# Performance work log

Hardware: AMD Instinct MI355X
Metric: run time of the kernel (lower is better)

The kernel has to match this reference:

```python
import jax, jax.numpy as jnp
import numpy as np

EMBED_DIM = 512
HEADS = 8
ATTN_DIM = EMBED_DIM // HEADS
PF_DIM = 2048
B, L = 4, 2048
LN_EPS = 1e-5


def _linear(x, W, b):
    # nn.Linear: x @ W.T + b, W is [out, in]
    return jnp.einsum('bld,od->blo', x, W) + b


def _layer_norm(x, g, b):
    mu = jnp.mean(x, axis=-1, keepdims=True)
    var = jnp.mean(jnp.square(x - mu), axis=-1, keepdims=True)
    return (x - mu) * jax.lax.rsqrt(var + LN_EPS) * g + b


def _qkv(src, Wq, bq, Wk, bk, Wv, bv):
    def split(t):
        Bb, Ll, _ = t.shape
        return t.reshape(Bb, Ll, HEADS, ATTN_DIM).transpose(0, 2, 1, 3)  # [B,H,L,Dh]
    return (split(_linear(src, Wq, bq)),
            split(_linear(src, Wk, bk)),
            split(_linear(src, Wv, bv)))


def _attention(inp, Q, K1, K2, V1, V2, Wo, bo, ln_g, ln_b, W1, b1, W2, b2):
    # non-softmax linear attention: (Q K1^T) V1 + (Q K2^T) V2
    attn = (jnp.einsum('bhqk,bhkd->bhqd', jnp.einsum('bhqd,bhkd->bhqk', Q, K1), V1)
            + jnp.einsum('bhqk,bhkd->bhqd', jnp.einsum('bhqd,bhkd->bhqk', Q, K2), V2))
    Bb = Q.shape[0]
    attn = attn.transpose(0, 2, 1, 3).reshape(Bb, -1, HEADS * ATTN_DIM)  # [B,L,D]
    x = _linear(attn, Wo, bo)
    x = _layer_norm(inp + x, ln_g, ln_b)          # dropout p=0 (eval)
    ff = _linear(jax.nn.relu(_linear(x, W1, b1)), W2, b2)
    x = _layer_norm(x + ff, ln_g, ln_b)
    return x


def setup_inputs() -> dict:
    key = jax.random.key(0)
    ks = jax.random.split(key, 16)
    s = 0.02
    return {
        'question': jax.random.normal(ks[0], (B, L, EMBED_DIM), jnp.float32),
        'query': jax.random.normal(ks[1], (B, L, EMBED_DIM), jnp.float32),
        'Wq': jax.random.normal(ks[2], (EMBED_DIM, EMBED_DIM), jnp.float32) * s,
        'bq': jnp.zeros((EMBED_DIM,), jnp.float32),
        'Wk': jax.random.normal(ks[3], (EMBED_DIM, EMBED_DIM), jnp.float32) * s,
        'bk': jnp.zeros((EMBED_DIM,), jnp.float32),
        'Wv': jax.random.normal(ks[4], (EMBED_DIM, EMBED_DIM), jnp.float32) * s,
        'bv': jnp.zeros((EMBED_DIM,), jnp.float32),
        'Wo': jax.random.normal(ks[5], (EMBED_DIM, EMBED_DIM), jnp.float32) * s,
        'bo': jnp.zeros((EMBED_DIM,), jnp.float32),
        'ln_g': jnp.ones((EMBED_DIM,), jnp.float32),
        'ln_b': jnp.zeros((EMBED_DIM,), jnp.float32),
        'W1': jax.random.normal(ks[6], (PF_DIM, EMBED_DIM), jnp.float32) * s,
        'b1': jnp.zeros((PF_DIM,), jnp.float32),
        'W2': jax.random.normal(ks[7], (EMBED_DIM, PF_DIM), jnp.float32) * s,
        'b2': jnp.zeros((EMBED_DIM,), jnp.float32),
    }


def reference(question, query, Wq, bq, Wk, bk, Wv, bv, Wo, bo, ln_g, ln_b, W1, b1, W2, b2):
    Q1, K1, V1 = _qkv(question, Wq, bq, Wk, bk, Wv, bv)
    Q2, K2, V2 = _qkv(query, Wq, bq, Wk, bk, Wv, bv)
    question_attn = _attention(question, Q1, K1, K2, V1, V2, Wo, bo, ln_g, ln_b, W1, b1, W2, b2)
    query_attn = _attention(query, Q2, K2, K1, V2, V1, Wo, bo, ln_g, ln_b, W1, b1, W2, b2)
    return jnp.concatenate([question_attn, query_attn], axis=-1)
```

## Files before the change

### kernel.cpp

```cpp
#include <hip/hip_runtime.h>
#include <stdint.h>


#define Bq 4
#define Lq 2048
#define Dq 512
#define PFq 2048
#define Mrows 16384
#define MiBu 1048576ull
#define NSLICE 16

typedef __attribute__((ext_vector_type(8))) short frag_ab;
typedef __attribute__((ext_vector_type(4))) float frag_cd;
typedef __attribute__((ext_vector_type(8))) unsigned short ushort8v;

__device__ __forceinline__ unsigned short f2b(float f) {
    union { float f; uint32_t u; } x; x.f = f;
    uint32_t r = x.u + 0x7fffu + ((x.u >> 16) & 1u);
    return (unsigned short)(r >> 16);
}
__device__ __forceinline__ float b2f(unsigned short u) {
    union { uint32_t u; float f; } x; x.u = ((uint32_t)u) << 16;
    return x.f;
}

#define GLD16(g, l)                                                              \
    __builtin_amdgcn_global_load_lds(                                            \
        (const __attribute__((address_space(1))) void*)(const void*)(g),         \
        (__attribute__((address_space(3))) void*)(void*)(l), 16, 0, 0)


#define STG(BUFOFS, REGOFS, GB, ROWOFS, TILE)                                    \
    { GLD16((GB) + (size_t)(ROWOFS) * 512 + (TILE) * 64,                         \
            Sh + (BUFOFS) + (REGOFS) + ld);                                      \
      GLD16((GB) + ((size_t)(ROWOFS) + 64) * 512 + (TILE) * 64,                  \
            Sh + (BUFOFS) + (REGOFS) + ld + 4096); }

#define VMW(N) asm volatile("s_waitcnt vmcnt(" #N ")" ::: "memory")

#define PHASE(CB, M0, LOADB, STAGE_STMT, WAIT_STMT)                              \
    {                                                                            \
        frag_ab a00 = *(const frag_ab*)&Sh[(CB) + (wm + (M0)*16 + lr) * 64 + xo0];      \
        frag_ab a01 = *(const frag_ab*)&Sh[(CB) + (wm + (M0)*16 + lr) * 64 + xo1];      \
        frag_ab a10 = *(const frag_ab*)&Sh[(CB) + (wm + (M0)*16 + 16 + lr) * 64 + xo0]; \
        frag_ab a11 = *(const frag_ab*)&Sh[(CB) + (wm + (M0)*16 + 16 + lr) * 64 + xo1]; \
        if (LOADB) {                                                             \
            _Pragma("unroll")                                                    \
            for (int j = 0; j < 4; ++j) {                                        \
                bf[j][0] = *(const frag_ab*)&Sh[(CB) + 16384 + (wn + j*16 + lr)*64 + xo0]; \
                bf[j][1] = *(const frag_ab*)&Sh[(CB) + 16384 + (wn + j*16 + lr)*64 + xo1]; \
            }                                                                    \
        }                                                                        \
        STAGE_STMT;                                                              \
        WAIT_STMT;                                                               \
        __builtin_amdgcn_sched_barrier(0);                                       \
        __builtin_amdgcn_s_barrier();                                            \
        asm volatile("s_waitcnt lgkmcnt(0)" ::: "memory");                       \
        __builtin_amdgcn_sched_barrier(0);                                       \
        __builtin_amdgcn_s_setprio(1);                                           \
        _Pragma("unroll")                                                        \
        for (int j = 0; j < 4; ++j) {                                            \
            acc[(M0)][j]   = __builtin_amdgcn_mfma_f32_16x16x32_bf16(a00, bf[j][0], acc[(M0)][j], 0,0,0);   \
            acc[(M0)][j]   = __builtin_amdgcn_mfma_f32_16x16x32_bf16(a01, bf[j][1], acc[(M0)][j], 0,0,0);   \
            acc[(M0)+1][j] = __builtin_amdgcn_mfma_f32_16x16x32_bf16(a10, bf[j][0], acc[(M0)+1][j], 0,0,0); \
            acc[(M0)+1][j] = __builtin_amdgcn_mfma_f32_16x16x32_bf16(a11, bf[j][1], acc[(M0)+1][j], 0,0,0); \
        }                                                                        \
        __builtin_amdgcn_s_setprio(0);                                           \
        __builtin_amdgcn_sched_barrier(0);                                       \
        __builtin_amdgcn_s_barrier();                                            \
        __builtin_amdgcn_sched_barrier(0);                                       \
    }

__global__ __launch_bounds__(512, 2) void gemm_256(
    const unsigned short* __restrict__ A, const unsigned short* __restrict__ Wt,
    const float* __restrict__ bias, unsigned short* __restrict__ outB,
    int M, int N, int relu)
{
    __shared__ __align__(16) unsigned short Sh[65536];
    const int tid = threadIdx.x;
    const int lane = tid & 63;
    const int w = tid >> 6;
    const int wm = (w >> 2) * 128;
    const int wn = (w & 3) * 64;
    const int lr = lane & 15;
    const int quad = lane >> 4;
    const int xo0 = ((quad ^ (lr & 7)) << 3);
    const int xo1 = (((4 | quad) ^ (lr & 7)) << 3);

    const int nwg = gridDim.x;
    const int b0 = blockIdx.x;
    const int bid = (b0 & 7) * (nwg >> 3) + (b0 >> 3);
    const int mb = M >> 8;
    const size_t bm = (size_t)(bid % mb) * 256;
    const size_t bn = (size_t)(bid / mb) * 256;

    const int ar = tid >> 3;
    const int sw = ((tid & 7) ^ (ar & 7)) << 3;
    const unsigned short* Ag = A  + (bm + ar) * (size_t)512 + sw;
    const unsigned short* Bg = Wt + (bn + ar) * (size_t)512 + sw;
    const int ld = tid * 8;

    frag_cd acc[8][4] = {};
    frag_ab bf[4][2];

    STG(0,     16384, Bg, 0,   0);
    STG(0,     24576, Bg, 128, 0);
    STG(0,     0,     Ag, 0,   0);
    STG(0,     8192,  Ag, 128, 0);
    STG(32768, 16384, Bg, 0,   1);
    STG(32768, 24576, Bg, 128, 1);
    VMW(4);
    __builtin_amdgcn_sched_barrier(0);
    __builtin_amdgcn_s_barrier();
    __builtin_amdgcn_sched_barrier(0);

    for (int I = 0; I < 3; ++I) {
        const int tb = 2 * I + 1, tc = 2 * I + 2, td = 2 * I + 3;
        PHASE(0,     0, 1, STG(32768, 0,     Ag, 0,   tb), (void)0);
        PHASE(0,     2, 0, STG(32768, 8192,  Ag, 128, tb), (void)0);
        PHASE(0,     4, 0, STG(0,     16384, Bg, 0,   tc), (void)0);
        PHASE(0,     6, 0, STG(0,     24576, Bg, 128, tc), VMW(4));
        PHASE(32768, 0, 1, STG(0,     0,     Ag, 0,   tc), (void)0);
        PHASE(32768, 2, 0, STG(0,     8192,  Ag, 128, tc), (void)0);
        PHASE(32768, 4, 0, STG(32768, 16384, Bg, 0,   td), (void)0);
        PHASE(32768, 6, 0, STG(32768, 24576, Bg, 128, td), VMW(4));
    }
    PHASE(0,     0, 1, STG(32768, 0,    Ag, 0,   7), (void)0);
    PHASE(0,     2, 0, STG(32768, 8192, Ag, 128, 7), (void)0);
    PHASE(0,     4, 0, (void)0, (void)0);
    PHASE(0,     6, 0, (void)0, VMW(0));
    PHASE(32768, 0, 1, (void)0, (void)0);
    PHASE(32768, 2, 0, (void)0, (void)0);
    PHASE(32768, 4, 0, (void)0, (void)0);
    PHASE(32768, 6, 0, (void)0, (void)0);

    float bv[4];
#pragma unroll
    for (int j = 0; j < 4; ++j) bv[j] = bias[(int)bn + wn + j * 16 + lr];
    unsigned short* Cs = Sh + w * 8192;
#pragma unroll
    for (int m = 0; m < 8; ++m)
#pragma unroll
        for (int j = 0; j < 4; ++j)
#pragma unroll
            for (int r = 0; r < 4; ++r) {
                float v = acc[m][j][r] + bv[j];
                if (relu) v = fmaxf(v, 0.f);
                Cs[(m * 16 + quad * 4 + r) * 64 + j * 16 + lr] = f2b(v);
            }
    const int rl = lane >> 3, c8 = (lane & 7) * 8;
#pragma unroll
    for (int k = 0; k < 16; ++k) {
        const int row = rl + k * 8;
        ushort8v val = *(const ushort8v*)&Cs[row * 64 + c8];
        *(ushort8v*)(outB + (size_t)(bm + wm + row) * N + bn + wn + c8) = val;
    }
}

__global__ __launch_bounds__(256) void gemm_res(
    const unsigned short* __restrict__ A, const unsigned short* __restrict__ Wt,
    const float* __restrict__ bias,
    const float* __restrict__ resA, const float* __restrict__ resB,
    unsigned short* __restrict__ outB, int M, int N, int K)
{
    __shared__ __align__(16) unsigned short Sh[128 * 64 + 64 * 64];
    unsigned short* At = Sh;
    unsigned short* Bt = Sh + 128 * 64;
    const int tid = threadIdx.x;
    const int lane = tid & 63;
    const int w = tid >> 6;
    const int wm = w * 32;
    const int lr = lane & 15;
    const int quad = lane >> 4;
    const size_t bm = (size_t)blockIdx.x * 128, bn = (size_t)blockIdx.y * 64;

    frag_cd acc[2][4] = {};

    const int ar = tid >> 3;
    const int acs = (((tid & 7) ^ (ar & 7)) << 3);
    const unsigned short* Ag = A  + (bm + ar) * (size_t)K + acs;
    const unsigned short* Bg = Wt + (bn + ar) * (size_t)K + acs;
    unsigned short* Asd = At + w * 512;
    unsigned short* Bsd = Bt + w * 512;

    for (int k0 = 0; k0 < K; k0 += 64) {
        __syncthreads();
#pragma unroll
        for (int i = 0; i < 4; ++i)
            GLD16(Ag + (size_t)(32 * i) * K + k0, Asd + i * 2048);
#pragma unroll
        for (int i = 0; i < 2; ++i)
            GLD16(Bg + (size_t)(32 * i) * K + k0, Bsd + i * 2048);
        __syncthreads();
#pragma unroll
        for (int kk = 0; kk < 2; ++kk) {
            frag_ab a[2], b[4];
#pragma unroll
            for (int i = 0; i < 2; ++i)
                a[i] = *(const frag_ab*)&At[(wm + i * 16 + lr) * 64 +
                                            ((((kk << 2) | quad) ^ (lr & 7)) << 3)];
#pragma unroll
            for (int j = 0; j < 4; ++j)
                b[j] = *(const frag_ab*)&Bt[(j * 16 + lr) * 64 +
                                            ((((kk << 2) | quad) ^ (lr & 7)) << 3)];
#pragma unroll
            for (int i = 0; i < 2; ++i)
#pragma unroll
                for (int j = 0; j < 4; ++j)
                    acc[i][j] = __builtin_amdgcn_mfma_f32_16x16x32_bf16(a[i], b[j], acc[i][j], 0, 0, 0);
        }
    }

    __syncthreads();
    unsigned short* Cs = Sh + w * 2048;
#pragma unroll
    for (int j = 0; j < 4; ++j) {
        const float bv = bias[(int)bn + j * 16 + lr];
#pragma unroll
        for (int i = 0; i < 2; ++i)
#pragma unroll
            for (int r = 0; r < 4; ++r)
                Cs[(i * 16 + quad * 4 + r) * 64 + j * 16 + lr] = f2b(acc[i][j][r] + bv);
    }
    const int rl = lane >> 3;
    const int c8 = (lane & 7) * 8;
#pragma unroll
    for (int k = 0; k < 4; ++k) {
        const int row = rl + k * 8;
        const int grow = (int)bm + wm + row;
        const size_t idx = (size_t)grow * N + bn + c8;
        ushort8v val = *(const ushort8v*)&Cs[row * 64 + c8];
        float vv[8];
#pragma unroll
        for (int t = 0; t < 8; ++t) vv[t] = b2f(val[t]);
        if (resA) {
            const float* rp = (grow < 8192) ? resA + idx : resB + idx - (size_t)8192 * N;
            float4 ra = *(const float4*)(rp);
            float4 rb = *(const float4*)(rp + 4);
            vv[0] += ra.x; vv[1] += ra.y; vv[2] += ra.z; vv[3] += ra.w;
            vv[4] += rb.x; vv[5] += rb.y; vv[6] += rb.z; vv[7] += rb.w;
        } else {
            ushort8v old = *(const ushort8v*)(outB + idx);
#pragma unroll
            for (int t = 0; t < 8; ++t) vv[t] += b2f(old[t]);
        }
        ushort8v o;
#pragma unroll
        for (int t = 0; t < 8; ++t) o[t] = f2b(vv[t]);
        *(ushort8v*)(outB + idx) = o;
    }
}

__global__ __launch_bounds__(256) void convert_all(
    const float* __restrict__ Wq, const float* __restrict__ Wk,
    const float* __restrict__ Wv, const float* __restrict__ Wo,
    const float* __restrict__ W1, const float* __restrict__ W2,
    const float* __restrict__ question, const float* __restrict__ query,
    const float* __restrict__ bqp, const float* __restrict__ bkp,
    const float* __restrict__ bvp,
    unsigned short* __restrict__ Wqkvb, unsigned short* __restrict__ Wob,
    unsigned short* __restrict__ W1b, unsigned short* __restrict__ W2b,
    unsigned short* __restrict__ Xb, float* __restrict__ bqkv)
{
    const int b = blockIdx.x;
    const float* src; unsigned short* dst; size_t off;
    if (b < 256)        { src = Wq; dst = Wqkvb;          off = (size_t)b * 1024; }
    else if (b < 512)   { src = Wk; dst = Wqkvb + 262144; off = (size_t)(b - 256) * 1024; }
    else if (b < 768)   { src = Wv; dst = Wqkvb + 524288; off = (size_t)(b - 512) * 1024; }
    else if (b < 1024)  { src = Wo; dst = Wob;            off = (size_t)(b - 768) * 1024; }
    else if (b < 2048)  { src = W1; dst = W1b;            off = (size_t)(b - 1024) * 1024; }
    else if (b < 3072)  { src = W2; dst = W2b;            off = (size_t)(b - 2048) * 1024; }
    else if (b < 7168)  { src = question; dst = Xb;       off = (size_t)(b - 3072) * 1024; }
    else if (b < 11264) { src = query; dst = Xb + 4194304; off = (size_t)(b - 7168) * 1024; }
    else {
        const int n = (b - 11264) * 256 + threadIdx.x;
        bqkv[n] = (n < 512) ? bqp[n] : (n < 1024) ? bkp[n - 512] : bvp[n - 1024];
        return;
    }
    const size_t idx = off + threadIdx.x * 4;
    float4 v = *(const float4*)(src + idx);
    ushort4 o;
    o.x = f2b(v.x); o.y = f2b(v.y); o.z = f2b(v.z); o.w = f2b(v.w);
    *(ushort4*)(dst + idx) = o;
}

__global__ __launch_bounds__(256) void s_kernel(
    const unsigned short* __restrict__ QKV, float* __restrict__ Spart)
{
    const int bh = blockIdx.x;
    const int sl = blockIdx.y;
    const int b = bh >> 3, h = bh & 7;
    const int pass = sl >> 3;
    const int l0 = (sl & 7) * 256;
    __shared__ float Ks[64][64];
    __shared__ float Vs[64][64];
    const int tid = threadIdx.x;
    const int tx = tid & 15, ty = tid >> 4;
    const int srow = tid >> 3;
    const int scol = (tid & 7) * 8;
    const size_t rowbase = (size_t)pass * 8192 + (size_t)b * Lq + l0;

    float acc[4][4] = {};

    for (int t0 = 0; t0 < 256; t0 += 64) {
        const unsigned short* kp0 = QKV + (rowbase + t0 + srow) * 1536 + 512 + h * 64 + scol;
        const unsigned short* kp1 = kp0 + (size_t)32 * 1536;
        ushort8v k0 = *(const ushort8v*)kp0;
        ushort8v v0 = *(const ushort8v*)(kp0 + 512);
        ushort8v k1 = *(const ushort8v*)kp1;
        ushort8v v1 = *(const ushort8v*)(kp1 + 512);
        __syncthreads();
#pragma unroll
        for (int e = 0; e < 8; ++e) {
            Ks[srow][scol + e]      = b2f(k0[e]);
            Vs[srow][scol + e]      = b2f(v0[e]);
            Ks[srow + 32][scol + e] = b2f(k1[e]);
            Vs[srow + 32][scol + e] = b2f(v1[e]);
        }
        __syncthreads();
#pragma unroll 4
        for (int rr = 0; rr < 64; ++rr) {
            const float4 kf = *(const float4*)&Ks[rr][ty * 4];
            const float4 vf = *(const float4*)&Vs[rr][tx * 4];
            acc[0][0] = fmaf(kf.x, vf.x, acc[0][0]);
            acc[0][1] = fmaf(kf.x, vf.y, acc[0][1]);
            acc[0][2] = fmaf(kf.x, vf.z, acc[0][2]);
            acc[0][3] = fmaf(kf.x, vf.w, acc[0][3]);
            acc[1][0] = fmaf(kf.y, vf.x, acc[1][0]);
            acc[1][1] = fmaf(kf.y, vf.y, acc[1][1]);
            acc[1][2] = fmaf(kf.y, vf.z, acc[1][2]);
            acc[1][3] = fmaf(kf.y, vf.w, acc[1][3]);
            acc[2][0] = fmaf(kf.z, vf.x, acc[2][0]);
            acc[2][1] = fmaf(kf.z, vf.y, acc[2][1]);
            acc[2][2] = fmaf(kf.z, vf.z, acc[2][2]);
            acc[2][3] = fmaf(kf.z, vf.w, acc[2][3]);
            acc[3][0] = fmaf(kf.w, vf.x, acc[3][0]);
            acc[3][1] = fmaf(kf.w, vf.y, acc[3][1]);
            acc[3][2] = fmaf(kf.w, vf.z, acc[3][2]);
            acc[3][3] = fmaf(kf.w, vf.w, acc[3][3]);
        }
    }

    float* Sp = Spart + ((size_t)bh * NSLICE + sl) * 4096;
#pragma unroll
    for (int i = 0; i < 4; ++i) {
        float4 o = make_float4(acc[i][0], acc[i][1], acc[i][2], acc[i][3]);
        *(float4*)(Sp + (ty * 4 + i) * 64 + tx * 4) = o;
    }
}

__global__ __launch_bounds__(256) void sbt_convert(
    const float* __restrict__ Spart, unsigned short* __restrict__ Sbt)
{
    const int bh = blockIdx.x;
    const int uo = blockIdx.y;
    const float* Sp = Spart + (size_t)bh * (NSLICE * 4096);
    unsigned short* Dp = Sbt + (size_t)bh * 4096;
    const int t = threadIdx.x;
#pragma unroll
    for (int u = 0; u < 4; ++u) {
        const int d = (uo * 4 + u) * 256 + t;
        float v = 0.f;
#pragma unroll
        for (int s = 0; s < NSLICE; ++s) v += Sp[(size_t)s * 4096 + d];
        const int row = d >> 6, col = d & 63;
        Dp[(row >> 5) * 2048 + col * 32 + (row & 31)] = f2b(v);
    }
}

__global__ __launch_bounds__(256) void attn_mfma(
    const unsigned short* __restrict__ QKV, const unsigned short* __restrict__ Sbt,
    unsigned short* __restrict__ Ob)
{
    __shared__ __align__(16) unsigned short Sh[2 * 128 * 32 + 2 * 64 * 32];
    unsigned short* At = Sh;
    unsigned short* Bt = Sh + 2 * 128 * 32;
    const int h = blockIdx.x;
    const int rbase = blockIdx.y * 128;
    const int b = (rbase >> 11) & 3;
    const int bh = b * 8 + h;
    const int tid = threadIdx.x;
    const int lane = tid & 63;
    const int w = tid >> 6;
    const int lr = lane & 15;
    const int quad = lane >> 4;

    {
        const int rloc = tid >> 2, c8 = (tid & 3) * 8;
#pragma unroll
        for (int it = 0; it < 4; ++it) {
            const int kk = it & 1, rh = it >> 1;
            const unsigned short* g = QKV +
                ((size_t)rbase + rh * 64 + rloc) * 1536 + h * 64 + kk * 32 + c8;
            GLD16(g, At + kk * 4096 + rh * 2048 + w * 512);
        }
        const unsigned short* Sg = Sbt + (size_t)bh * 4096 + tid * 8;
#pragma unroll
        for (int bi = 0; bi < 2; ++bi)
            GLD16(Sg + bi * 2048, Bt + bi * 2048 + w * 512);
    }
    __syncthreads();

    frag_cd acc[2][4] = {};
#pragma unroll
    for (int kk = 0; kk < 2; ++kk) {
        frag_ab a[2], bfr[4];
#pragma unroll
        for (int i = 0; i < 2; ++i)
            a[i] = *(const frag_ab*)&At[kk * 4096 + (w * 32 + i * 16 + lr) * 32 + quad * 8];
#pragma unroll
        for (int j = 0; j < 4; ++j)
            bfr[j] = *(const frag_ab*)&Bt[kk * 2048 + (j * 16 + lr) * 32 + quad * 8];
#pragma unroll
        for (int i = 0; i < 2; ++i)
#pragma unroll
            for (int j = 0; j < 4; ++j)
                acc[i][j] = __builtin_amdgcn_mfma_f32_16x16x32_bf16(a[i], bfr[j], acc[i][j], 0, 0, 0);
    }

    __syncthreads();
    unsigned short* Cs = Sh + w * 2048;
#pragma unroll
    for (int i = 0; i < 2; ++i)
#pragma unroll
        for (int j = 0; j < 4; ++j)
#pragma unroll
            for (int r = 0; r < 4; ++r)
                Cs[(i * 16 + quad * 4 + r) * 64 + j * 16 + lr] = f2b(acc[i][j][r]);
    const int rl = lane >> 3;
    const int c8o = (lane & 7) * 8;
#pragma unroll
    for (int k = 0; k < 4; ++k) {
        const int row = rl + k * 8;
        ushort8v val = *(const ushort8v*)&Cs[row * 64 + c8o];
        *(ushort8v*)(Ob + (size_t)(rbase + w * 32 + row) * 512 + h * 64 + c8o) = val;
    }
}

__global__ __launch_bounds__(256) void ln_b16_inplace(
    unsigned short* __restrict__ Y, const float* __restrict__ g,
    const float* __restrict__ bta)
{
    __shared__ float part[8];
    const int row = blockIdx.x;
    const int t = threadIdx.x;
    const int w = t >> 6;
    unsigned short* yr = Y + (size_t)row * Dq;
    const float v0 = b2f(yr[t]), v1 = b2f(yr[t + 256]);
    float s = v0 + v1;
#pragma unroll
    for (int off = 32; off; off >>= 1) s += __shfl_xor(s, off, 64);
    if ((t & 63) == 0) part[w] = s;
    __syncthreads();
    const float mean = (part[0] + part[1] + part[2] + part[3]) * (1.f / Dq);
    const float d0 = v0 - mean, d1 = v1 - mean;
    float q = d0 * d0 + d1 * d1;
#pragma unroll
    for (int off = 32; off; off >>= 1) q += __shfl_xor(q, off, 64);
    if ((t & 63) == 0) part[4 + w] = q;
    __syncthreads();
    const float rstd = rsqrtf((part[4] + part[5] + part[6] + part[7]) * (1.f / Dq) + 1e-5f);
    yr[t] = f2b(d0 * rstd * g[t] + bta[t]);
    yr[t + 256] = f2b(d1 * rstd * g[t + 256] + bta[t + 256]);
}

__global__ __launch_bounds__(256) void ln_b16_out(
    const unsigned short* __restrict__ Y, const float* __restrict__ g,
    const float* __restrict__ bta, float* __restrict__ out)
{
    __shared__ float part[8];
    const int row = blockIdx.x;
    const int t = threadIdx.x;
    const int w = t >> 6;
    const unsigned short* yr = Y + (size_t)row * Dq;
    const float v0 = b2f(yr[t]), v1 = b2f(yr[t + 256]);
    float s = v0 + v1;
#pragma unroll
    for (int off = 32; off; off >>= 1) s += __shfl_xor(s, off, 64);
    if ((t & 63) == 0) part[w] = s;
    __syncthreads();
    const float mean = (part[0] + part[1] + part[2] + part[3]) * (1.f / Dq);
    const float d0 = v0 - mean, d1 = v1 - mean;
    float q = d0 * d0 + d1 * d1;
#pragma unroll
    for (int off = 32; off; off >>= 1) q += __shfl_xor(q, off, 64);
    if ((t & 63) == 0) part[4 + w] = q;
    __syncthreads();
    const float rstd = rsqrtf((part[4] + part[5] + part[6] + part[7]) * (1.f / Dq) + 1e-5f);
    const int half = row >> 13, br = row & 8191;
    float* orow = out + (size_t)br * 1024 + half * 512;
    orow[t] = d0 * rstd * g[t] + bta[t];
    orow[t + 256] = d1 * rstd * g[t + 256] + bta[t + 256];
}

extern "C" void kernel_launch(void* const* d_in, const int* in_sizes, int n_in,
                              void* d_out, int out_size, void* d_ws, size_t ws_size,
                              hipStream_t stream)
{
    const float* question = (const float*)d_in[0];
    const float* query    = (const float*)d_in[1];
    const float* Wq = (const float*)d_in[2];  const float* bqp = (const float*)d_in[3];
    const float* Wk = (const float*)d_in[4];  const float* bkp = (const float*)d_in[5];
    const float* Wv = (const float*)d_in[6];  const float* bvp = (const float*)d_in[7];
    const float* Wo = (const float*)d_in[8];  const float* bo  = (const float*)d_in[9];
    const float* ln_g = (const float*)d_in[10]; const float* ln_b = (const float*)d_in[11];
    const float* W1 = (const float*)d_in[12]; const float* b1 = (const float*)d_in[13];
    const float* W2 = (const float*)d_in[14]; const float* b2 = (const float*)d_in[15];
    float* out = (float*)d_out;
    char* ws = (char*)d_ws;

    unsigned short* QKVb  = (unsigned short*)(ws);
    unsigned short* attnb = (unsigned short*)(ws + 48 * MiBu);
    float* Spart          = (float*)(ws + 48 * MiBu);
    unsigned short* Xb    = (unsigned short*)(ws + 64 * MiBu);
    unsigned short* xbuf  = (unsigned short*)(ws + 64 * MiBu);
    unsigned short* hb    = (unsigned short*)(ws);
    char* wp = ws + 80 * MiBu + 524288;
    unsigned short* Wqkvb = (unsigned short*)wp;  wp += 1536 * 512 * 2;
    unsigned short* Wob   = (unsigned short*)wp;  wp += 512 * 512 * 2;
    unsigned short* W1b   = (unsigned short*)wp;  wp += 2048 * 512 * 2;
    unsigned short* W2b   = (unsigned short*)wp;  wp += 512 * 2048 * 2;
    unsigned short* Sbt   = (unsigned short*)wp;  wp += 32 * 4096 * 2;
    float* bqkv           = (float*)wp;

    dim3 blk(256);

    convert_all<<<11270, blk, 0, stream>>>(Wq, Wk, Wv, Wo, W1, W2, question, query,
                                           bqp, bkp, bvp,
                                           Wqkvb, Wob, W1b, W2b, Xb, bqkv);

    gemm_256<<<dim3(384), dim3(512), 0, stream>>>(Xb, Wqkvb, bqkv, QKVb,
                                                  Mrows, 1536, 0);

    s_kernel<<<dim3(32, NSLICE), blk, 0, stream>>>(QKVb, Spart);
    sbt_convert<<<dim3(32, 4), blk, 0, stream>>>(Spart, Sbt);
    attn_mfma<<<dim3(8, 128), blk, 0, stream>>>(QKVb, Sbt, attnb);

    gemm_res<<<dim3(128, 8), blk, 0, stream>>>(attnb, Wob, bo, question, query,
                                               xbuf, Mrows, 512, 512);

    ln_b16_inplace<<<Mrows, blk, 0, stream>>>(xbuf, ln_g, ln_b);

    gemm_256<<<dim3(512), dim3(512), 0, stream>>>(xbuf, W1b, b1, hb,
                                                  Mrows, PFq, 1);

    gemm_res<<<dim3(128, 8), blk, 0, stream>>>(hb, W2b, b2, nullptr, nullptr,
                                               xbuf, Mrows, 512, PFq);

    ln_b16_out<<<Mrows, blk, 0, stream>>>(xbuf, ln_g, ln_b, out);
}
```

Baseline: 319.9 us.

## Replace residual GEMM with 256x128 double-buffered pipelined MFMA kernel

The simple 128x64 residual GEMM, which synchronised twice per K step, is replaced by a 256x128-tile kernel with 512 threads. It uses the same double-buffered global_load_lds staging and phase pipeline as the main gemm_256 kernel, plus an XCD-aware block swizzle. The STG macro gains a K-stride argument so the pipeline works for both K=512 and K=2048. The aim is more data reuse per tile and loads overlapped with MFMA work, at the cost of fewer blocks (256) and more LDS per block.

```diff
diff --git a/kernel.cpp b/kernel.cpp
--- a/kernel.cpp
+++ b/kernel.cpp
@@ -29,11 +29,10 @@
         (const __attribute__((address_space(1))) void*)(const void*)(g),         \
         (__attribute__((address_space(3))) void*)(void*)(l), 16, 0, 0)
 
-
-#define STG(BUFOFS, REGOFS, GB, ROWOFS, TILE)                                    \
-    { GLD16((GB) + (size_t)(ROWOFS) * 512 + (TILE) * 64,                         \
+#define STG(BUFOFS, REGOFS, GB, ROWOFS, TILE, KS)                                \
+    { GLD16((GB) + (size_t)(ROWOFS) * (KS) + (TILE) * 64,                        \
             Sh + (BUFOFS) + (REGOFS) + ld);                                      \
-      GLD16((GB) + ((size_t)(ROWOFS) + 64) * 512 + (TILE) * 64,                  \
+      GLD16((GB) + ((size_t)(ROWOFS) + 64) * (KS) + (TILE) * 64,                 \
             Sh + (BUFOFS) + (REGOFS) + ld + 4096); }
 
 #define VMW(N) asm volatile("s_waitcnt vmcnt(" #N ")" ::: "memory")
@@ -103,12 +102,12 @@
     frag_cd acc[8][4] = {};
     frag_ab bf[4][2];
 
-    STG(0,     16384, Bg, 0,   0);
-    STG(0,     24576, Bg, 128, 0);
-    STG(0,     0,     Ag, 0,   0);
-    STG(0,     8192,  Ag, 128, 0);
-    STG(32768, 16384, Bg, 0,   1);
-    STG(32768, 24576, Bg, 128, 1);
+    STG(0,     16384, Bg, 0,   0, 512);
+    STG(0,     24576, Bg, 128, 0, 512);
+    STG(0,     0,     Ag, 0,   0, 512);
+    STG(0,     8192,  Ag, 128, 0, 512);
+    STG(32768, 16384, Bg, 0,   1, 512);
+    STG(32768, 24576, Bg, 128, 1, 512);
     VMW(4);
     __builtin_amdgcn_sched_barrier(0);
     __builtin_amdgcn_s_barrier();
@@ -116,17 +115,17 @@
 
     for (int I = 0; I < 3; ++I) {
         const int tb = 2 * I + 1, tc = 2 * I + 2, td = 2 * I + 3;
-        PHASE(0,     0, 1, STG(32768, 0,     Ag, 0,   tb), (void)0);
-        PHASE(0,     2, 0, STG(32768, 8192,  Ag, 128, tb), (void)0);
-        PHASE(0,     4, 0, STG(0,     16384, Bg, 0,   tc), (void)0);
-        PHASE(0,     6, 0, STG(0,     24576, Bg, 128, tc), VMW(4));
-        PHASE(32768, 0, 1, STG(0,     0,     Ag, 0,   tc), (void)0);
-        PHASE(32768, 2, 0, STG(0,     8192,  Ag, 128, tc), (void)0);
-        PHASE(32768, 4, 0, STG(32768, 16384, Bg, 0,   td), (void)0);
-        PHASE(32768, 6, 0, STG(32768, 24576, Bg, 128, td), VMW(4));
-    }
-    PHASE(0,     0, 1, STG(32768, 0,    Ag, 0,   7), (void)0);
-    PHASE(0,     2, 0, STG(32768, 8192, Ag, 128, 7), (void)0);
+        PHASE(0,     0, 1, STG(32768, 0,     Ag, 0,   tb, 512), (void)0);
+        PHASE(0,     2, 0, STG(32768, 8192,  Ag, 128, tb, 512), (void)0);
+        PHASE(0,     4, 0, STG(0,     16384, Bg, 0,   tc, 512), (void)0);
+        PHASE(0,     6, 0, STG(0,     24576, Bg, 128, tc, 512), VMW(4));
+        PHASE(32768, 0, 1, STG(0,     0,     Ag, 0,   tc, 512), (void)0);
+        PHASE(32768, 2, 0, STG(0,     8192,  Ag, 128, tc, 512), (void)0);
+        PHASE(32768, 4, 0, STG(32768, 16384, Bg, 0,   td, 512), (void)0);
+        PHASE(32768, 6, 0, STG(32768, 24576, Bg, 128, td, 512), VMW(4));
+    }
+    PHASE(0,     0, 1, STG(32768, 0,    Ag, 0,   7, 512), (void)0);
+    PHASE(0,     2, 0, STG(32768, 8192, Ag, 128, 7, 512), (void)0);
     PHASE(0,     4, 0, (void)0, (void)0);
     PHASE(0,     6, 0, (void)0, VMW(0));
     PHASE(32768, 0, 1, (void)0, (void)0);
@@ -157,84 +156,85 @@
     }
 }
 
-__global__ __launch_bounds__(256) void gemm_res(
+__global__ __launch_bounds__(512, 2) void gemm_res256(
     const unsigned short* __restrict__ A, const unsigned short* __restrict__ Wt,
     const float* __restrict__ bias,
     const float* __restrict__ resA, const float* __restrict__ resB,
-    unsigned short* __restrict__ outB, int M, int N, int K)
-{
-    __shared__ __align__(16) unsigned short Sh[128 * 64 + 64 * 64];
-    unsigned short* At = Sh;
-    unsigned short* Bt = Sh + 128 * 64;
+    unsigned short* __restrict__ outB, int K)
+{
+    __shared__ __align__(16) unsigned short Sh[49152];
     const int tid = threadIdx.x;
     const int lane = tid & 63;
     const int w = tid >> 6;
-    const int wm = w * 32;
+    const int wm = (w >> 1) * 64;
+    const int wn = (w & 1) * 64;
     const int lr = lane & 15;
     const int quad = lane >> 4;
-    const size_t bm = (size_t)blockIdx.x * 128, bn = (size_t)blockIdx.y * 64;
-
-    frag_cd acc[2][4] = {};
+    const int xo0 = ((quad ^ (lr & 7)) << 3);
+    const int xo1 = (((4 | quad) ^ (lr & 7)) << 3);
+
+    const int b0 = blockIdx.x;
+    const int bid = (b0 & 7) * 32 + (b0 >> 3);
+    const size_t bm = (size_t)(bid & 63) * 256;
+    const size_t bn = (size_t)(bid >> 6) * 128;
 
     const int ar = tid >> 3;
-    const int acs = (((tid & 7) ^ (ar & 7)) << 3);
-    const unsigned short* Ag = A  + (bm + ar) * (size_t)K + acs;
-    const unsigned short* Bg = Wt + (bn + ar) * (size_t)K + acs;
-    unsigned short* Asd = At + w * 512;
-    unsigned short* Bsd = Bt + w * 512;
-
-    for (int k0 = 0; k0 < K; k0 += 64) {
-        __syncthreads();
-#pragma unroll
-        for (int i = 0; i < 4; ++i)
-            GLD16(Ag + (size_t)(32 * i) * K + k0, Asd + i * 2048);
-#pragma unroll
-        for (int i = 0; i < 2; ++i)
-            GLD16(Bg + (size_t)(32 * i) * K + k0, Bsd + i * 2048);
-        __syncthreads();
-#pragma unroll
-        for (int kk = 0; kk < 2; ++kk) {
-            frag_ab a[2], b[4];
-#pragma unroll
-            for (int i = 0; i < 2; ++i)
-                a[i] = *(const frag_ab*)&At[(wm + i * 16 + lr) * 64 +
-                                            ((((kk << 2) | quad) ^ (lr & 7)) << 3)];
-#pragma unroll
-            for (int j = 0; j < 4; ++j)
-                b[j] = *(const frag_ab*)&Bt[(j * 16 + lr) * 64 +
-                                            ((((kk << 2) | quad) ^ (lr & 7)) << 3)];
-#pragma unroll
-            for (int i = 0; i < 2; ++i)
-#pragma unroll
-                for (int j = 0; j < 4; ++j)
-                    acc[i][j] = __builtin_amdgcn_mfma_f32_16x16x32_bf16(a[i], b[j], acc[i][j], 0, 0, 0);
-        }
-    }
-
-    __syncthreads();
-    unsigned short* Cs = Sh + w * 2048;
-#pragma unroll
-    for (int j = 0; j < 4; ++j) {
-        const float bv = bias[(int)bn + j * 16 + lr];
-#pragma unroll
-        for (int i = 0; i < 2; ++i)
+    const int sw = ((tid & 7) ^ (ar & 7)) << 3;
+    const unsigned short* Ag = A  + (bm + ar) * (size_t)K + sw;
+    const unsigned short* Bg = Wt + (bn + ar) * (size_t)K + sw;
+    const int ld = tid * 8;
+
+    frag_cd acc[4][4] = {};
+    frag_ab bf[4][2];
+
+    STG(0,     16384, Bg, 0,   0, K);
+    STG(0,     0,     Ag, 0,   0, K);
+    STG(0,     8192,  Ag, 128, 0, K);
+    STG(24576, 16384, Bg, 0,   1, K);
+    VMW(2);
+    __builtin_amdgcn_sched_barrier(0);
+    __builtin_amdgcn_s_barrier();
+    __builtin_amdgcn_sched_barrier(0);
+
+    const int nIter = K >> 7;
+    for (int I = 0; I < nIter - 1; ++I) {
+        const int tb = 2 * I + 1, tc = 2 * I + 2, td = 2 * I + 3;
+        PHASE(0,     0, 1, { STG(24576, 0, Ag, 0, tb, K); STG(24576, 8192, Ag, 128, tb, K); }, (void)0);
+        PHASE(0,     2, 0, STG(0, 16384, Bg, 0, tc, K), VMW(2));
+        PHASE(24576, 0, 1, { STG(0, 0, Ag, 0, tc, K); STG(0, 8192, Ag, 128, tc, K); }, (void)0);
+        PHASE(24576, 2, 0, STG(24576, 16384, Bg, 0, td, K), VMW(2));
+    }
+    {
+        const int tb = (K >> 6) - 1;
+        PHASE(0,     0, 1, { STG(24576, 0, Ag, 0, tb, K); STG(24576, 8192, Ag, 128, tb, K); }, (void)0);
+        PHASE(0,     2, 0, (void)0, VMW(0));
+        PHASE(24576, 0, 1, (void)0, (void)0);
+        PHASE(24576, 2, 0, (void)0, (void)0);
+    }
+
+    float bv[4];
+#pragma unroll
+    for (int j = 0; j < 4; ++j) bv[j] = bias[(int)bn + wn + j * 16 + lr];
+    unsigned short* Cs = Sh + w * 4096;
+#pragma unroll
+    for (int m = 0; m < 4; ++m)
+#pragma unroll
+        for (int j = 0; j < 4; ++j)
 #pragma unroll
             for (int r = 0; r < 4; ++r)
-                Cs[(i * 16 + quad * 4 + r) * 64 + j * 16 + lr] = f2b(acc[i][j][r] + bv);
-    }
-    const int rl = lane >> 3;
-    const int c8 = (lane & 7) * 8;
-#pragma unroll
-    for (int k = 0; k < 4; ++k) {
+                Cs[(m * 16 + quad * 4 + r) * 64 + j * 16 + lr] = f2b(acc[m][j][r] + bv[j]);
+    const int rl = lane >> 3, c8 = (lane & 7) * 8;
+#pragma unroll
+    for (int k = 0; k < 8; ++k) {
         const int row = rl + k * 8;
         const int grow = (int)bm + wm + row;
-        const size_t idx = (size_t)grow * N + bn + c8;
+        const size_t idx = (size_t)grow * 512 + bn + wn + c8;
         ushort8v val = *(const ushort8v*)&Cs[row * 64 + c8];
         float vv[8];
 #pragma unroll
         for (int t = 0; t < 8; ++t) vv[t] = b2f(val[t]);
         if (resA) {
-            const float* rp = (grow < 8192) ? resA + idx : resB + idx - (size_t)8192 * N;
+            const float* rp = (grow < 8192) ? resA + idx : resB + idx - (size_t)8192 * 512;
             float4 ra = *(const float4*)(rp);
             float4 rb = *(const float4*)(rp + 4);
             vv[0] += ra.x; vv[1] += ra.y; vv[2] += ra.z; vv[3] += ra.w;
@@ -536,16 +536,16 @@
     sbt_convert<<<dim3(32, 4), blk, 0, stream>>>(Spart, Sbt);
     attn_mfma<<<dim3(8, 128), blk, 0, stream>>>(QKVb, Sbt, attnb);
 
-    gemm_res<<<dim3(128, 8), blk, 0, stream>>>(attnb, Wob, bo, question, query,
-                                               xbuf, Mrows, 512, 512);
+    gemm_res256<<<dim3(256), dim3(512), 0, stream>>>(attnb, Wob, bo,
+                                                     question, query, xbuf, 512);
 
     ln_b16_inplace<<<Mrows, blk, 0, stream>>>(xbuf, ln_g, ln_b);
 
     gemm_256<<<dim3(512), dim3(512), 0, stream>>>(xbuf, W1b, b1, hb,
                                                   Mrows, PFq, 1);
 
-    gemm_res<<<dim3(128, 8), blk, 0, stream>>>(hb, W2b, b2, nullptr, nullptr,
-                                               xbuf, Mrows, 512, PFq);
+    gemm_res256<<<dim3(256), dim3(512), 0, stream>>>(hb, W2b, b2,
+                                                     nullptr, nullptr, xbuf, 2048);
 
     ln_b16_out<<<Mrows, blk, 0, stream>>>(xbuf, ln_g, ln_b, out);
 }
```

After: 317.8 us. No clear change (-0.6%).
